# Kernel tuning notes

Hardware: AMD Instinct MI355X
Metric: run time of the kernel (lower is better)

Reference implementation:

```python
import jax, jax.numpy as jnp
import numpy as np

B, D = 8192, 1024

def setup_inputs() -> dict:
    key = jax.random.key(0)
    ks = jax.random.split(key, 5)
    scale = 1.0 / np.sqrt(D)
    return {
        "x": jax.random.normal(ks[0], (B, D), dtype=jnp.float32),
        "h": jax.random.normal(ks[1], (B, D), dtype=jnp.float32),
        "c": jax.random.normal(ks[2], (B, D), dtype=jnp.float32),
        # gate order: [input, forget, output, candidate]
        "Wx": jax.random.normal(ks[3], (4, D, D), dtype=jnp.float32) * scale,
        "Wh": jax.random.normal(ks[4], (4, D, D), dtype=jnp.float32) * scale,
    }

def reference(x, h, c, Wx, Wh):
    # two batched GEMMs covering all 8 projections: [B,D] x [4,D,D] -> [4,B,D]
    gx = jnp.einsum('bd,gdk->gbk', x, Wx)
    gh = jnp.einsum('bd,gdk->gbk', h, Wh)
    g = gx + gh
    i = jax.nn.sigmoid(g[0])
    f = jax.nn.sigmoid(g[1])
    o = jax.nn.sigmoid(g[2])
    u = jnp.tanh(g[3])
    c_t = i * u + f * c
    h_t = o * jnp.tanh(c_t)
    return (h_t, c_t)
```

## Files before the change

kernel.cpp:

```cpp
#include <hip/hip_runtime.h>
#include <hip/hip_bf16.h>
#include <cstdint>


#define LDS_TOTAL 131072

typedef __attribute__((ext_vector_type(8))) short bf16x8;
typedef __attribute__((ext_vector_type(16))) float f32x16;
typedef __attribute__((ext_vector_type(4))) unsigned int u32x4;

static __device__ __forceinline__ unsigned short f2bf(float f) {
  union { float f; unsigned int u; } v; v.f = f;
  unsigned int u = v.u;
  unsigned int r = (u + 0x7FFFu + ((u >> 16) & 1u)) >> 16;
  return (unsigned short)r;
}

static __device__ __forceinline__ void load16(const void* gp, void* lp) {
  __builtin_amdgcn_global_load_lds(
      (const __attribute__((address_space(1))) void*)gp,
      (__attribute__((address_space(3))) void*)lp, 16, 0, 0);
}

static __device__ __forceinline__ float sigmoid_f(float x) {
  return 1.0f / (1.0f + __expf(-x));
}
static __device__ __forceinline__ float tanh_f(float x) {
  float e = __expf(-2.0f * fabsf(x));
  float r = (1.0f - e) / (1.0f + e);
  return copysignf(r, x);
}

__global__ __launch_bounds__(256) void pack_a_kernel(
    const float* __restrict__ x, const float* __restrict__ h,
    unsigned short* __restrict__ Ap) {
  __shared__ float tile[64][65];
  const int b0 = (blockIdx.x >> 5) << 6;
  const int k0 = (blockIdx.x & 31) << 6;
  const float* src; int ks;
  if (k0 < 1024) { src = x; ks = k0; } else { src = h; ks = k0 - 1024; }
  const int r = threadIdx.x >> 4;
  const int c4 = (threadIdx.x & 15) << 2;
  #pragma unroll
  for (int s = 0; s < 4; ++s) {
    float4 v = *(const float4*)(src + (size_t)(b0 + s * 16 + r) * 1024 + ks + c4);
    tile[s * 16 + r][c4 + 0] = v.x; tile[s * 16 + r][c4 + 1] = v.y;
    tile[s * 16 + r][c4 + 2] = v.z; tile[s * 16 + r][c4 + 3] = v.w;
  }
  __syncthreads();
  #pragma unroll
  for (int i = 0; i < 2; ++i) {
    int cc = i * 256 + threadIdx.x;
    int kb = cc >> 6, bb = cc & 63;
    union { unsigned short s[8]; u32x4 v; } o;
    #pragma unroll
    for (int e = 0; e < 8; ++e) o.s[e] = f2bf(tile[bb][kb * 8 + e]);
    *(u32x4*)(Ap + ((size_t)((k0 >> 3) + kb) * 8192 + b0 + bb) * 8) = o.v;
  }
}

__global__ __launch_bounds__(256) void prep_w_kernel(
    const float* __restrict__ Wx, const float* __restrict__ Wh,
    unsigned short* __restrict__ Wt2) {
  __shared__ float tile[64][65];
  const int g = blockIdx.x >> 9;
  const int kt = (blockIdx.x >> 4) & 31;
  const int nt = blockIdx.x & 15;
  const int k0 = kt << 6, n0 = nt << 6;
  const float* W; int ks;
  if (k0 < 1024) { W = Wx + (size_t)g * 1048576; ks = k0; }
  else           { W = Wh + (size_t)g * 1048576; ks = k0 - 1024; }
  const int r = threadIdx.x >> 4;
  const int c4 = (threadIdx.x & 15) << 2;
  #pragma unroll
  for (int s = 0; s < 4; ++s) {
    float4 v = *(const float4*)(W + (size_t)(ks + s * 16 + r) * 1024 + n0 + c4);
    tile[s * 16 + r][c4 + 0] = v.x; tile[s * 16 + r][c4 + 1] = v.y;
    tile[s * 16 + r][c4 + 2] = v.z; tile[s * 16 + r][c4 + 3] = v.w;
  }
  __syncthreads();
  #pragma unroll
  for (int i = 0; i < 2; ++i) {
    int cc = i * 256 + threadIdx.x;
    int kb = cc >> 6, nn = cc & 63;
    union { unsigned short s[8]; u32x4 v; } o;
    #pragma unroll
    for (int e = 0; e < 8; ++e) o.s[e] = f2bf(tile[kb * 8 + e][nn]);
    *(u32x4*)(Wt2 + ((size_t)((k0 >> 3) + kb) * 4096 + g * 1024 + n0 + nn) * 8) = o.v;
  }
}

#define VMW(n) asm volatile("s_waitcnt vmcnt(" #n ")" ::: "memory")

__global__ __launch_bounds__(512, 2) void lstm_gemm_kernel(
    const unsigned short* __restrict__ Ap,
    const unsigned short* __restrict__ Wt2,
    const float* __restrict__ cprev,
    float* __restrict__ out) {
  extern __shared__ char lds[];
  const int tid = threadIdx.x;
  const int l = tid & 63;
  const int w = tid >> 6;
  const int wr = w >> 1;
  const int wc = w & 1;
  const int bid = blockIdx.x;
  const int xcd = bid & 7;
  const int cc = bid >> 3;
  const int nt = xcd * 2 + (cc >> 5);
  const int mt = cc & 31;
  const int m0 = mt << 8;
  const int n0 = nt << 6;

  char* const buf0 = lds;
  char* const buf1 = lds + 65536;

  f32x16 acc[2][4];
  #pragma unroll
  for (int mf = 0; mf < 2; ++mf)
    #pragma unroll
    for (int g = 0; g < 4; ++g) acc[mf][g] = (f32x16)0.0f;

  const int ln = l & 31;
  const int hl = l >> 5;

  const int aBase = hl * 4096 + (wr * 64 + ln) * 16;
  const int bBase = 32768 + hl * 1024 + (wc * 32 + ln) * 16;

  const unsigned short* const gA =
      Ap + (size_t)(tid >> 8) * 65536 + (size_t)(m0 + (tid & 255)) * 8;
  const unsigned short* const gB =
      Wt2 + (size_t)((tid >> 6) & 1) * 32768 +
      (size_t)((tid >> 7) * 1024 + n0 + (tid & 63)) * 8;
  const int dA = (tid & ~63) << 4;
  const int dB = 32768 + ((tid & ~63) << 4);

  auto stA = [&](char* buf, int j, int t) {
    load16(gA + (size_t)(t * 8 + j * 2) * 65536, buf + j * 8192 + dA);
  };
  auto stB = [&](char* buf, int j, int t) {
    load16(gB + (size_t)(t * 8 + j * 2) * 32768, buf + j * 8192 + dB);
  };

  bf16x8 aR[2], bR[4];
  auto rd = [&](const char* bufc, int p) {
    const char* pb = bufc + p * 8192;
    aR[0] = *(const bf16x8*)(pb + aBase);
    aR[1] = *(const bf16x8*)(pb + aBase + 512);
    bR[0] = *(const bf16x8*)(pb + bBase);
    bR[1] = *(const bf16x8*)(pb + bBase + 2048);
    bR[2] = *(const bf16x8*)(pb + bBase + 4096);
    bR[3] = *(const bf16x8*)(pb + bBase + 6144);
  };
  auto post = [&]() {
    __builtin_amdgcn_s_barrier();
    asm volatile("s_waitcnt lgkmcnt(0)" ::: "memory");
    __builtin_amdgcn_s_setprio(1);
    #pragma unroll
    for (int mf = 0; mf < 2; ++mf)
      #pragma unroll
      for (int g = 0; g < 4; ++g)
        acc[mf][g] = __builtin_amdgcn_mfma_f32_32x32x16_bf16(
            aR[mf], bR[g], acc[mf][g], 0, 0, 0);
    __builtin_amdgcn_s_setprio(0);
    __builtin_amdgcn_s_barrier();
  };

  #pragma unroll
  for (int j = 0; j < 4; ++j) { stA(buf0, j, 0); stB(buf0, j, 0); }
  #pragma unroll
  for (int j = 0; j < 3; ++j) { stA(buf1, j, 1); stB(buf1, j, 1); }
  VMW(6);
  __builtin_amdgcn_s_barrier();

  #pragma unroll 1
  for (int t = 0; t < 30; ++t) {
    char* bufc = lds + ((t & 1) << 16);
    char* bufn = lds + (((t + 1) & 1) << 16);
    rd(bufc, 0); stA(bufn, 3, t + 1); stB(bufn, 3, t + 1); VMW(12); post();
    rd(bufc, 1); stA(bufc, 0, t + 2); stB(bufc, 0, t + 2); VMW(12); post();
    rd(bufc, 2); stA(bufc, 1, t + 2); stB(bufc, 1, t + 2); VMW(12); post();
    rd(bufc, 3); stA(bufc, 2, t + 2); stB(bufc, 2, t + 2); VMW(12); post();
  }
  rd(buf0, 0); stA(buf1, 3, 31); stB(buf1, 3, 31); VMW(12); post();
  rd(buf0, 1); VMW(10); post();
  rd(buf0, 2); VMW(8);  post();
  rd(buf0, 3); VMW(6);  post();
  rd(buf1, 0); VMW(4); post();
  rd(buf1, 1); VMW(2); post();
  rd(buf1, 2); VMW(0); post();
  rd(buf1, 3);         post();

  const int colB = n0 + wc * 32 + ln;
  #pragma unroll
  for (int mf = 0; mf < 2; ++mf) {
    #pragma unroll
    for (int r = 0; r < 16; ++r) {
      int row = m0 + wr * 64 + mf * 32 + (r & 3) + ((r >> 2) << 3) + (hl << 2);
      float gi = acc[mf][0][r];
      float gf = acc[mf][1][r];
      float go = acc[mf][2][r];
      float gu = acc[mf][3][r];
      float i_ = sigmoid_f(gi);
      float f_ = sigmoid_f(gf);
      float o_ = sigmoid_f(go);
      float u_ = tanh_f(gu);
      size_t idx = (size_t)row * 1024 + colB;
      float ct = i_ * u_ + f_ * cprev[idx];
      float ht = o_ * tanh_f(ct);
      out[idx] = ht;
      out[8388608 + idx] = ct;
    }
  }
}

extern "C" void kernel_launch(void* const* d_in, const int* in_sizes, int n_in,
                              void* d_out, int out_size, void* d_ws, size_t ws_size,
                              hipStream_t stream) {
  const float* x  = (const float*)d_in[0];
  const float* h  = (const float*)d_in[1];
  const float* c  = (const float*)d_in[2];
  const float* Wx = (const float*)d_in[3];
  const float* Wh = (const float*)d_in[4];
  float* out = (float*)d_out;

  unsigned short* Ap  = (unsigned short*)d_ws;
  unsigned short* Wt2 = (unsigned short*)((char*)d_ws + 33554432);

  hipFuncSetAttribute((const void*)lstm_gemm_kernel,
                      hipFuncAttributeMaxDynamicSharedMemorySize, LDS_TOTAL);

  pack_a_kernel<<<4096, 256, 0, stream>>>(x, h, Ap);
  prep_w_kernel<<<2048, 256, 0, stream>>>(Wx, Wh, Wt2);
  lstm_gemm_kernel<<<dim3(512), dim3(512), LDS_TOTAL, stream>>>(Ap, Wt2, c, out);
}
```

Baseline: 168.5 us.

## Halve GEMM block tile, use triple-buffered LDS with register double-buffered fragments

Shrinks each GEMM block from 512 to 256 threads with an M tile of 128 rows, doubling the grid to 1024 blocks. The old two-buffer, four-phase LDS scheme becomes a three-slot ring of 24KB slots (72KB total), so two blocks can share a CU. Each slot holds a 32-wide K step. LDS fragments for the next step are read into a second register set while MFMAs run on the current one. The aim is more occupancy and better overlap of loads with math, at the cost of a full vmcnt(0) wait each step and more B traffic per output.

```diff
diff --git a/kernel.cpp b/kernel.cpp
--- a/kernel.cpp
+++ b/kernel.cpp
@@ -3,7 +3,7 @@
 #include <cstdint>
 
 
-#define LDS_TOTAL 131072
+#define LDS_TOTAL 73728
 
 typedef __attribute__((ext_vector_type(8))) short bf16x8;
 typedef __attribute__((ext_vector_type(16))) float f32x16;
@@ -91,8 +91,9 @@
 }
 
 #define VMW(n) asm volatile("s_waitcnt vmcnt(" #n ")" ::: "memory")
-
-__global__ __launch_bounds__(512, 2) void lstm_gemm_kernel(
+#define BAR() __builtin_amdgcn_s_barrier()
+
+__global__ __launch_bounds__(256, 2) void lstm_gemm_kernel(
     const unsigned short* __restrict__ Ap,
     const unsigned short* __restrict__ Wt2,
     const float* __restrict__ cprev,
@@ -106,13 +107,10 @@
   const int bid = blockIdx.x;
   const int xcd = bid & 7;
   const int cc = bid >> 3;
-  const int nt = xcd * 2 + (cc >> 5);
-  const int mt = cc & 31;
-  const int m0 = mt << 8;
+  const int nt = xcd * 2 + (cc >> 6);
+  const int mt = cc & 63;
+  const int m0 = mt << 7;
   const int n0 = nt << 6;
-
-  char* const buf0 = lds;
-  char* const buf1 = lds + 65536;
 
   f32x16 acc[2][4];
   #pragma unroll
@@ -123,72 +121,82 @@
   const int ln = l & 31;
   const int hl = l >> 5;
 
-  const int aBase = hl * 4096 + (wr * 64 + ln) * 16;
-  const int bBase = 32768 + hl * 1024 + (wc * 32 + ln) * 16;
+  const int aOff = hl * 2048 + (wr * 64 + ln) * 16;
+  const int bOff = 8192 + hl * 4096 + (wc * 32 + ln) * 16;
 
   const unsigned short* const gA =
-      Ap + (size_t)(tid >> 8) * 65536 + (size_t)(m0 + (tid & 255)) * 8;
+      Ap + (size_t)((tid >> 7) * 8192 + m0 + (tid & 127)) * 8;
   const unsigned short* const gB =
-      Wt2 + (size_t)((tid >> 6) & 1) * 32768 +
-      (size_t)((tid >> 7) * 1024 + n0 + (tid & 63)) * 8;
+      Wt2 + (size_t)(((tid >> 6) & 3) * 1024 + n0 + (tid & 63)) * 8;
   const int dA = (tid & ~63) << 4;
-  const int dB = 32768 + ((tid & ~63) << 4);
-
-  auto stA = [&](char* buf, int j, int t) {
-    load16(gA + (size_t)(t * 8 + j * 2) * 65536, buf + j * 8192 + dA);
+  const int dB = 8192 + dA;
+
+  auto stage = [&](int bo, int t) {
+    const unsigned short* a0 = gA + (size_t)t * 262144;
+    load16(a0,          lds + bo + dA);
+    load16(a0 + 131072, lds + bo + dA + 4096);
+    const unsigned short* b0 = gB + (size_t)t * 131072;
+    load16(b0,          lds + bo + dB);
+    load16(b0 + 32768,  lds + bo + dB + 4096);
+    load16(b0 + 65536,  lds + bo + dB + 8192);
+    load16(b0 + 98304,  lds + bo + dB + 12288);
   };
-  auto stB = [&](char* buf, int j, int t) {
-    load16(gB + (size_t)(t * 8 + j * 2) * 32768, buf + j * 8192 + dB);
-  };
-
-  bf16x8 aR[2], bR[4];
-  auto rd = [&](const char* bufc, int p) {
-    const char* pb = bufc + p * 8192;
-    aR[0] = *(const bf16x8*)(pb + aBase);
-    aR[1] = *(const bf16x8*)(pb + aBase + 512);
-    bR[0] = *(const bf16x8*)(pb + bBase);
-    bR[1] = *(const bf16x8*)(pb + bBase + 2048);
-    bR[2] = *(const bf16x8*)(pb + bBase + 4096);
-    bR[3] = *(const bf16x8*)(pb + bBase + 6144);
-  };
-  auto post = [&]() {
-    __builtin_amdgcn_s_barrier();
-    asm volatile("s_waitcnt lgkmcnt(0)" ::: "memory");
-    __builtin_amdgcn_s_setprio(1);
-    #pragma unroll
-    for (int mf = 0; mf < 2; ++mf)
-      #pragma unroll
-      for (int g = 0; g < 4; ++g)
-        acc[mf][g] = __builtin_amdgcn_mfma_f32_32x32x16_bf16(
-            aR[mf], bR[g], acc[mf][g], 0, 0, 0);
-    __builtin_amdgcn_s_setprio(0);
-    __builtin_amdgcn_s_barrier();
-  };
-
-  #pragma unroll
-  for (int j = 0; j < 4; ++j) { stA(buf0, j, 0); stB(buf0, j, 0); }
-  #pragma unroll
-  for (int j = 0; j < 3; ++j) { stA(buf1, j, 1); stB(buf1, j, 1); }
+
+  bf16x8 eA[2][2], eB[2][4], oA[2][2], oB[2][4];
+
+#define RD_SET(SA, SB, bo) do {                                   \
+    const char* base_ = lds + (bo);                               \
+    SA[0][0] = *(const bf16x8*)(base_ + aOff);                    \
+    SA[0][1] = *(const bf16x8*)(base_ + aOff + 512);              \
+    SA[1][0] = *(const bf16x8*)(base_ + aOff + 4096);             \
+    SA[1][1] = *(const bf16x8*)(base_ + aOff + 4608);             \
+    SB[0][0] = *(const bf16x8*)(base_ + bOff);                    \
+    SB[0][1] = *(const bf16x8*)(base_ + bOff + 1024);             \
+    SB[0][2] = *(const bf16x8*)(base_ + bOff + 2048);             \
+    SB[0][3] = *(const bf16x8*)(base_ + bOff + 3072);             \
+    SB[1][0] = *(const bf16x8*)(base_ + bOff + 8192);             \
+    SB[1][1] = *(const bf16x8*)(base_ + bOff + 9216);             \
+    SB[1][2] = *(const bf16x8*)(base_ + bOff + 10240);            \
+    SB[1][3] = *(const bf16x8*)(base_ + bOff + 11264);            \
+  } while (0)
+
+#define MM_SET(SA, SB) do {                                       \
+    _Pragma("unroll")                                             \
+    for (int r_ = 0; r_ < 2; ++r_)                                \
+      _Pragma("unroll")                                           \
+      for (int mf_ = 0; mf_ < 2; ++mf_)                           \
+        _Pragma("unroll")                                         \
+        for (int g_ = 0; g_ < 4; ++g_)                            \
+          acc[mf_][g_] = __builtin_amdgcn_mfma_f32_32x32x16_bf16( \
+              SA[r_][mf_], SB[r_][g_], acc[mf_][g_], 0, 0, 0);    \
+  } while (0)
+
+  int bo0 = 0, bo1 = 24576, bo2 = 49152;
+  stage(bo0, 0);
+  stage(bo1, 1);
   VMW(6);
-  __builtin_amdgcn_s_barrier();
+  BAR();
+  RD_SET(eA, eB, bo0);
 
   #pragma unroll 1
-  for (int t = 0; t < 30; ++t) {
-    char* bufc = lds + ((t & 1) << 16);
-    char* bufn = lds + (((t + 1) & 1) << 16);
-    rd(bufc, 0); stA(bufn, 3, t + 1); stB(bufn, 3, t + 1); VMW(12); post();
-    rd(bufc, 1); stA(bufc, 0, t + 2); stB(bufc, 0, t + 2); VMW(12); post();
-    rd(bufc, 2); stA(bufc, 1, t + 2); stB(bufc, 1, t + 2); VMW(12); post();
-    rd(bufc, 3); stA(bufc, 2, t + 2); stB(bufc, 2, t + 2); VMW(12); post();
-  }
-  rd(buf0, 0); stA(buf1, 3, 31); stB(buf1, 3, 31); VMW(12); post();
-  rd(buf0, 1); VMW(10); post();
-  rd(buf0, 2); VMW(8);  post();
-  rd(buf0, 3); VMW(6);  post();
-  rd(buf1, 0); VMW(4); post();
-  rd(buf1, 1); VMW(2); post();
-  rd(buf1, 2); VMW(0); post();
-  rd(buf1, 3);         post();
+  for (int tt = 0; tt < 31; ++tt) {
+    const int t = 2 * tt;
+    VMW(0); BAR();
+    RD_SET(oA, oB, bo1);
+    stage(bo2, t + 2);
+    MM_SET(eA, eB);
+    { int tmp = bo0; bo0 = bo1; bo1 = bo2; bo2 = tmp; }
+    VMW(0); BAR();
+    RD_SET(eA, eB, bo1);
+    stage(bo2, t + 3);
+    MM_SET(oA, oB);
+    { int tmp = bo0; bo0 = bo1; bo1 = bo2; bo2 = tmp; }
+  }
+  VMW(0); BAR();
+  RD_SET(oA, oB, bo1);
+  MM_SET(eA, eB);
+  BAR();
+  MM_SET(oA, oB);
 
   const int colB = n0 + wc * 32 + ln;
   #pragma unroll
@@ -211,6 +219,8 @@
       out[8388608 + idx] = ct;
     }
   }
+#undef RD_SET
+#undef MM_SET
 }
 
 extern "C" void kernel_launch(void* const* d_in, const int* in_sizes, int n_in,
@@ -231,5 +241,5 @@
 
   pack_a_kernel<<<4096, 256, 0, stream>>>(x, h, Ap);
   prep_w_kernel<<<2048, 256, 0, stream>>>(Wx, Wh, Wt2);
-  lstm_gemm_kernel<<<dim3(512), dim3(512), LDS_TOTAL, stream>>>(Ap, Wt2, c, out);
-}
+  lstm_gemm_kernel<<<dim3(1024), dim3(256), LDS_TOTAL, stream>>>(Ap, Wt2, c, out);
+}
```

Result: no change. 171.8 us (+1.9%).
